# Optimization experiments

Hardware: AMD Instinct MI355X
Metric: run time of the kernel (lower is better)

## Reference

```python
import jax, jax.numpy as jnp
import numpy as np

N = 50000      # nodes per graph
E = 1600000    # edges per graph
D_IN = 128
D_HID = 128
D_OUT = 128
D_GF = 128
N_LAYERS = 3   # input->hid, hid->hid (hidden_layer=1), hid->out


def setup_inputs() -> dict:
    key = jax.random.key(0)
    ks = jax.random.split(key, 24)
    inp = {
        "feat_p": jax.random.normal(ks[0], (N, D_IN), jnp.float32),
        "src_p": jax.random.randint(ks[1], (E,), 0, N, jnp.int32),
        "dst_p": jax.random.randint(ks[2], (E,), 0, N, jnp.int32),
        "feat_s": jax.random.normal(ks[3], (N, D_IN), jnp.float32),
        "src_s": jax.random.randint(ks[4], (E,), 0, N, jnp.int32),
        "dst_s": jax.random.randint(ks[5], (E,), 0, N, jnp.int32),
    }
    dims = [(D_IN, D_HID), (D_HID, D_HID), (D_HID, D_OUT)]
    for i, (di, do) in enumerate(dims):
        inp[f"W{i}"] = jax.random.normal(ks[6 + 2 * i], (di, do), jnp.float32) * 0.05
        inp[f"b{i}"] = jnp.zeros((do,), jnp.float32)
    inp["Wr"] = jax.random.normal(ks[14], (D_OUT, D_GF), jnp.float32) * 0.05
    inp["br"] = jnp.zeros((D_GF,), jnp.float32)
    inp["Wm1"] = jax.random.normal(ks[15], (2 * D_GF, D_GF), jnp.float32) * 0.05
    inp["bm1"] = jnp.zeros((D_GF,), jnp.float32)
    inp["Wm2"] = jax.random.normal(ks[16], (D_GF, 1), jnp.float32) * 0.05
    inp["bm2"] = jnp.zeros((1,), jnp.float32)
    return inp


def _gcn_stack(feat, src, dst, layers):
    """Stacked GCN: mean over incoming messages, then linear.
    NOTE: the original SingleGCN never applies its ReLU (bug preserved)."""
    n = feat.shape[0]
    deg = jax.ops.segment_sum(jnp.ones_like(src, feat.dtype), dst, num_segments=n)
    inv_deg = (1.0 / jnp.maximum(deg, 1.0))[:, None]  # [N,1]
    h = feat
    for W, b in layers:
        msg = h[src]                                           # [E,d] gather
        agg = jax.ops.segment_sum(msg, dst, num_segments=n)    # [N,d] scatter-add
        h = (agg * inv_deg) @ W + b                            # mean + linear
    return h


def reference(feat_p, src_p, dst_p, feat_s, src_s, dst_s,
              W0, b0, W1, b1, W2, b2, Wr, br, Wm1, bm1, Wm2, bm2):
    layers = [(W0, b0), (W1, b1), (W2, b2)]
    h_p = _gcn_stack(feat_p, src_p, dst_p, layers)
    h_s = _gcn_stack(feat_s, src_s, dst_s, layers)
    # ReadOut: mean over nodes -> linear -> sigmoid
    g_p = jax.nn.sigmoid(jnp.mean(h_p, axis=0) @ Wr + br)  # [D_GF]
    g_s = jax.nn.sigmoid(jnp.mean(h_s, axis=0) @ Wr + br)
    # Match: concat -> linear -> linear -> sigmoid
    c = jnp.concatenate([g_p, g_s], axis=-1)               # [2*D_GF]
    d = (c @ Wm1 + bm1) @ Wm2 + bm2                        # [1]
    return jax.nn.sigmoid(d)
```

## Files before the change

### kernel.cpp

```cpp
#include <hip/hip_runtime.h>
#include <math.h>

#define D 128
#define HQ 4
#define BB 64


__global__ __launch_bounds__(1024, 8) void scan_scatter(
        const int* __restrict__ tgt_p, const int* __restrict__ oth_p,
        const int* __restrict__ tgt_s, const int* __restrict__ oth_s,
        const float* __restrict__ w, float* __restrict__ rep,
        float* __restrict__ zbase, int zcount,
        int E, int N, int HN, float scale) {
    const int b = blockIdx.x, h = blockIdx.y, g = blockIdx.z;
    const int* tgt = g ? tgt_s : tgt_p;
    const int* oth = g ? oth_s : oth_p;
    const float* wg = w ? (w + (size_t)g * N) : nullptr;

    if (zbase && b == 0 && h == 0 && g == 0)
        for (int i = threadIdx.x; i < zcount; i += 1024) zbase[i] = 0.f;

    extern __shared__ float lds[];
    {
        float4 z = make_float4(0.f, 0.f, 0.f, 0.f);
        float4* l4 = (float4*)lds;
        for (int i = threadIdx.x; i < HN / 4; i += 1024) l4[i] = z;
    }
    __syncthreads();

    const int lo = h * HN;
    const int hi = min(lo + HN, N);
    const unsigned span = (unsigned)(hi - lo);
    int C = (E + BB - 1) / BB;
    C = (C + 7) & ~7;
    const int e0 = b * C;
    const int e1 = min(e0 + C, E);

    for (int e = e0 + (int)threadIdx.x * 8; e < e1; e += 1024 * 8) {
        if (e + 8 <= e1) {
            int4 ta = *(const int4*)(tgt + e);
            int4 tb = *(const int4*)(tgt + e + 4);
            int idx[8] = {ta.x, ta.y, ta.z, ta.w, tb.x, tb.y, tb.z, tb.w};
            bool hit[8];
            #pragma unroll
            for (int k = 0; k < 8; ++k) hit[k] = (unsigned)(idx[k] - lo) < span;
            if (wg) {
                int4 oa = *(const int4*)(oth + e);
                int4 ob = *(const int4*)(oth + e + 4);
                int od[8] = {oa.x, oa.y, oa.z, oa.w, ob.x, ob.y, ob.z, ob.w};
                float val[8];
                #pragma unroll
                for (int k = 0; k < 8; ++k) val[k] = hit[k] ? wg[od[k]] : 0.f;
                #pragma unroll
                for (int k = 0; k < 8; ++k)
                    if (hit[k]) atomicAdd(&lds[idx[k] - lo], val[k] * scale);
            } else {
                #pragma unroll
                for (int k = 0; k < 8; ++k)
                    if (hit[k]) atomicAdd(&lds[idx[k] - lo], 1.0f);
            }
        } else {
            for (int e2 = e; e2 < e1; ++e2) {
                int t = tgt[e2];
                if ((unsigned)(t - lo) < span) {
                    float v = wg ? wg[oth[e2]] * scale : 1.0f;
                    atomicAdd(&lds[t - lo], v);
                }
            }
        }
    }
    __syncthreads();

    float* dst = rep + (((size_t)g * HQ + h) * BB + b) * HN;
    float4* d4 = (float4*)dst;
    const float4* l4 = (const float4*)lds;
    for (int i = threadIdx.x; i < HN / 4; i += 1024) d4[i] = l4[i];
}

__global__ __launch_bounds__(256) void reduce_inv(
        const float* __restrict__ rep, float* __restrict__ inv,
        int N, int HN) {
    const int lane = threadIdx.x & 63;
    const int s = threadIdx.x >> 6;
    const int i = (blockIdx.x * 64 + lane) * 4;
    const int bps = BB >> 2;
    float4 u = make_float4(0.f, 0.f, 0.f, 0.f);
    if (i < 2 * N) {
        int g = (i < N) ? 0 : 1;
        int n = i - g * N;
        int h = n / HN, l = n - h * HN;
        const float* base = rep + (((size_t)g * HQ + h) * BB + (size_t)s * bps) * HN + l;
        #pragma unroll 16
        for (int b = 0; b < bps; b++) {
            float4 v = *(const float4*)(base + (size_t)b * HN);
            u.x += v.x; u.y += v.y; u.z += v.z; u.w += v.w;
        }
    }
    __shared__ float4 sm[256];
    sm[threadIdx.x] = u;
    __syncthreads();
    if (s == 0 && i < 2 * N) {
        float4 a = sm[lane], b4 = sm[64 + lane], c = sm[128 + lane], d = sm[192 + lane];
        float4 r;
        r.x = 1.0f / fmaxf(a.x + b4.x + c.x + d.x, 1.0f);
        r.y = 1.0f / fmaxf(a.y + b4.y + c.y + d.y, 1.0f);
        r.z = 1.0f / fmaxf(a.z + b4.z + c.z + d.z, 1.0f);
        r.w = 1.0f / fmaxf(a.w + b4.w + c.w + d.w, 1.0f);
        *(float4*)(inv + i) = r;
    }
}

__global__ __launch_bounds__(256) void reduce_u(
        const float* __restrict__ rep, const float* __restrict__ inv,
        float* __restrict__ out_u, float* __restrict__ out_w,
        float* __restrict__ sums, int s_idx, int N, int HN) {
    const int lane = threadIdx.x & 63;
    const int s = threadIdx.x >> 6;
    const int i = (blockIdx.x * 64 + lane) * 4;
    const int bps = BB >> 2;
    float4 u = make_float4(0.f, 0.f, 0.f, 0.f);
    if (i < 2 * N) {
        int g = (i < N) ? 0 : 1;
        int n = i - g * N;
        int h = n / HN, l = n - h * HN;
        const float* base = rep + (((size_t)g * HQ + h) * BB + (size_t)s * bps) * HN + l;
        #pragma unroll 16
        for (int b = 0; b < bps; b++) {
            float4 v = *(const float4*)(base + (size_t)b * HN);
            u.x += v.x; u.y += v.y; u.z += v.z; u.w += v.w;
        }
    }
    __shared__ float4 sm[256];
    __shared__ float s0[64], s1[64];
    sm[threadIdx.x] = u;
    __syncthreads();
    if (s == 0) {
        float tp = 0.f, ts = 0.f;
        if (i < 2 * N) {
            float4 a = sm[lane], b4 = sm[64 + lane], c = sm[128 + lane], d = sm[192 + lane];
            float4 uu;
            uu.x = a.x + b4.x + c.x + d.x;
            uu.y = a.y + b4.y + c.y + d.y;
            uu.z = a.z + b4.z + c.z + d.z;
            uu.w = a.w + b4.w + c.w + d.w;
            if (out_u) *(float4*)(out_u + i) = uu;
            if (out_w) {
                float4 iv = *(const float4*)(inv + i);
                *(float4*)(out_w + i) =
                    make_float4(uu.x * iv.x, uu.y * iv.y, uu.z * iv.z, uu.w * iv.w);
            }
            float t = uu.x + uu.y + uu.z + uu.w;
            if (i < N) tp = t; else ts = t;
        }
        s0[lane] = tp; s1[lane] = ts;
    }
    __syncthreads();
    if (sums) {
        for (int st = 32; st > 0; st >>= 1) {
            if ((int)threadIdx.x < st) {
                s0[threadIdx.x] += s0[threadIdx.x + st];
                s1[threadIdx.x] += s1[threadIdx.x + st];
            }
            __syncthreads();
        }
        if (threadIdx.x == 0) {
            if (s0[0] != 0.f) atomicAdd(&sums[0 * 2 + s_idx], s0[0]);
            if (s1[0] != 0.f) atomicAdd(&sums[1 * 2 + s_idx], s1[0]);
        }
    }
}

__global__ __launch_bounds__(256) void featsum_kernel(
        const float* __restrict__ feat_p, const float* __restrict__ feat_s,
        const float* __restrict__ u3, float* __restrict__ fpart2,
        int N, int rpb) {
    const int g = blockIdx.y;
    const float* feat = g ? feat_s : feat_p;
    const float* u = u3 + (size_t)g * N;
    const int col4 = threadIdx.x & 31;
    const int rgrp = threadIdx.x >> 5;
    const int r0 = blockIdx.x * rpb;
    const int r1 = min(r0 + rpb, N);

    const float4* f4 = (const float4*)feat;
    float4 acc = make_float4(0.f, 0.f, 0.f, 0.f);
    for (int n = r0 + rgrp * 4; n + 3 < r1; n += 32) {
        float4 uu = *(const float4*)(u + n);
        float4 v0 = f4[(size_t)n * 32 + col4];
        float4 v1 = f4[(size_t)(n + 1) * 32 + col4];
        float4 v2 = f4[(size_t)(n + 2) * 32 + col4];
        float4 v3 = f4[(size_t)(n + 3) * 32 + col4];
        acc.x += uu.x * v0.x + uu.y * v1.x + uu.z * v2.x + uu.w * v3.x;
        acc.y += uu.x * v0.y + uu.y * v1.y + uu.z * v2.y + uu.w * v3.y;
        acc.z += uu.x * v0.z + uu.y * v1.z + uu.z * v2.z + uu.w * v3.z;
        acc.w += uu.x * v0.w + uu.y * v1.w + uu.z * v2.w + uu.w * v3.w;
    }
    __shared__ float4 smem[256];
    smem[threadIdx.x] = acc;
    __syncthreads();
    if (rgrp == 0) {
        float4 t = smem[col4];
        #pragma unroll
        for (int k = 1; k < 8; k++) {
            float4 o = smem[k * 32 + col4];
            t.x += o.x; t.y += o.y; t.z += o.z; t.w += o.w;
        }
        float* dst = fpart2 + ((size_t)g * 16 + (blockIdx.x & 15)) * 128 + col4 * 4;
        atomicAdd(dst + 0, t.x);
        atomicAdd(dst + 1, t.y);
        atomicAdd(dst + 2, t.z);
        atomicAdd(dst + 3, t.w);
    }
}

__global__ __launch_bounds__(512) void final_kernel(
        const float* __restrict__ fpart2,
        const float* __restrict__ sums,
        const float* __restrict__ W0, const float* __restrict__ b0,
        const float* __restrict__ W1, const float* __restrict__ b1,
        const float* __restrict__ W2, const float* __restrict__ b2,
        const float* __restrict__ Wr, const float* __restrict__ br,
        const float* __restrict__ Wm1, const float* __restrict__ bm1,
        const float* __restrict__ Wm2, const float* __restrict__ bm2,
        float* __restrict__ out) {
    __shared__ float x[128];
    __shared__ float part[4][128];
    __shared__ float rvec[256];
    __shared__ float Avec[128], Bvec[128];
    __shared__ float gv[256];
    const int tid = threadIdx.x;
    const int j = tid & 127;
    const int h = tid >> 7;

    auto mv128 = [&](const float* __restrict__ W, float* __restrict__ buf) {
        float p = 0.f;
        const float* Wp = W + (size_t)(h * 32) * 128 + j;
        #pragma unroll
        for (int i = 0; i < 32; ++i) p += buf[h * 32 + i] * Wp[(size_t)i * 128];
        part[h][j] = p;
        __syncthreads();
        if (h == 0) buf[j] = part[0][j] + part[1][j] + part[2][j] + part[3][j];
        __syncthreads();
    };

    if (tid < 256) {
        int g = tid >> 7;
        const float* fp = fpart2 + (size_t)g * 2048 + (tid & 127);
        float rv = 0.f;
        #pragma unroll
        for (int b = 0; b < 16; ++b) rv += fp[(size_t)b * 128];
        rvec[tid] = rv;
    }
    __syncthreads();

    if (tid < 128) x[tid] = b0[tid];
    __syncthreads();
    mv128(W1, x);
    mv128(W2, x);
    if (tid < 128) Avec[tid] = x[tid];
    __syncthreads();
    if (tid < 128) x[tid] = b1[tid];
    __syncthreads();
    mv128(W2, x);
    if (tid < 128) Bvec[tid] = x[tid];
    __syncthreads();

    for (int g = 0; g < 2; ++g) {
        const float s1 = sums[g * 2 + 0];
        const float s2 = sums[g * 2 + 1];
        if (tid < 128) x[tid] = rvec[g * 128 + tid];
        __syncthreads();
        mv128(W0, x);
        mv128(W1, x);
        mv128(W2, x);
        if (tid < 128) x[tid] += s2 * Avec[tid] + s1 * Bvec[tid] + b2[tid];
        __syncthreads();
        mv128(Wr, x);
        if (tid < 128) gv[g * 128 + tid] = 1.0f / (1.0f + expf(-(x[tid] + br[tid])));
        __syncthreads();
    }

    {
        float p = 0.f;
        const float* Wp = Wm1 + (size_t)(h * 64) * 128 + j;
        #pragma unroll
        for (int i = 0; i < 64; ++i) p += gv[h * 64 + i] * Wp[(size_t)i * 128];
        part[h][j] = p;
        __syncthreads();
        if (h == 0)
            part[0][j] = (part[0][j] + part[1][j] + part[2][j] + part[3][j] + bm1[j]) * Wm2[j];
        __syncthreads();
        if (tid < 64) part[0][tid] += part[0][tid + 64];
        __syncthreads();
        if (tid < 32) part[0][tid] += part[0][tid + 32];
        __syncthreads();
        if (tid < 16) part[0][tid] += part[0][tid + 16];
        __syncthreads();
        if (tid < 8) part[0][tid] += part[0][tid + 8];
        __syncthreads();
        if (tid < 4) part[0][tid] += part[0][tid + 4];
        __syncthreads();
        if (tid < 2) part[0][tid] += part[0][tid + 2];
        __syncthreads();
        if (tid == 0) out[0] = 1.0f / (1.0f + expf(-(part[0][0] + part[0][1] + bm2[0])));
    }
}

extern "C" void kernel_launch(void* const* d_in, const int* in_sizes, int n_in,
                              void* d_out, int out_size, void* d_ws, size_t ws_size,
                              hipStream_t stream) {
    const float* feat_p = (const float*)d_in[0];
    const int*   src_p  = (const int*)d_in[1];
    const int*   dst_p  = (const int*)d_in[2];
    const float* feat_s = (const float*)d_in[3];
    const int*   src_s  = (const int*)d_in[4];
    const int*   dst_s  = (const int*)d_in[5];
    const float* W0 = (const float*)d_in[6];
    const float* b0 = (const float*)d_in[7];
    const float* W1 = (const float*)d_in[8];
    const float* b1 = (const float*)d_in[9];
    const float* W2 = (const float*)d_in[10];
    const float* b2 = (const float*)d_in[11];
    const float* Wr = (const float*)d_in[12];
    const float* br = (const float*)d_in[13];
    const float* Wm1 = (const float*)d_in[14];
    const float* bm1 = (const float*)d_in[15];
    const float* Wm2 = (const float*)d_in[16];
    const float* bm2 = (const float*)d_in[17];
    float* out = (float*)d_out;

    const int N = in_sizes[0] / D;
    const int E = in_sizes[1];
    const int N2 = 2 * N;

    int HN = (N + HQ - 1) / HQ;
    HN = (HN + 3) & ~3;
    const int FB = 256;
    const int rpb = (((N + FB - 1) / FB) + 3) & ~3;

    float* ws     = (float*)d_ws;
    float* sums   = ws;
    float* fpart2 = ws + 16;
    float* inv    = fpart2 + 2 * 16 * 128;
    float* w1     = inv + N2;
    float* w2     = w1 + N2;
    float* u3     = w2 + N2;
    float* rep    = u3 + N2;

    const dim3 sgrid(BB, HQ, 2);
    const size_t lds_bytes = (size_t)HN * sizeof(float);
    const int gQ = (N2 / 4 + 63) / 64;
    const float u0 = 1.0f / (float)N;
    const int zcount = 16 + 2 * 16 * 128;

    scan_scatter<<<sgrid, 1024, lds_bytes, stream>>>(dst_p, nullptr, dst_s, nullptr,
                                                     nullptr, rep, sums, zcount,
                                                     E, N, HN, 1.0f);
    reduce_inv<<<gQ, 256, 0, stream>>>(rep, inv, N, HN);

    scan_scatter<<<sgrid, 1024, lds_bytes, stream>>>(src_p, dst_p, src_s, dst_s,
                                                     inv, rep, nullptr, 0,
                                                     E, N, HN, u0);
    reduce_u<<<gQ, 256, 0, stream>>>(rep, inv, nullptr, w1, sums, 0, N, HN);

    scan_scatter<<<sgrid, 1024, lds_bytes, stream>>>(src_p, dst_p, src_s, dst_s,
                                                     w1, rep, nullptr, 0,
                                                     E, N, HN, 1.0f);
    reduce_u<<<gQ, 256, 0, stream>>>(rep, inv, nullptr, w2, sums, 1, N, HN);

    scan_scatter<<<sgrid, 1024, lds_bytes, stream>>>(src_p, dst_p, src_s, dst_s,
                                                     w2, rep, nullptr, 0,
                                                     E, N, HN, 1.0f);
    reduce_u<<<gQ, 256, 0, stream>>>(rep, inv, u3, nullptr, nullptr, 0, N, HN);

    featsum_kernel<<<dim3(FB, 2), 256, 0, stream>>>(feat_p, feat_s, u3, fpart2, N, rpb);

    final_kernel<<<1, 512, 0, stream>>>(fpart2, sums, W0, b0, W1, b1, W2, b2,
                                        Wr, br, Wm1, bm1, Wm2, bm2, out);
}
```

Before: 284.9 us.

## Compute degrees with global atomics and halve node partitions in scatter

The degree count now uses a dedicated global-atomic kernel plus a small inverse kernel, replacing the LDS-partitioned scan_scatter pass and its reduce_inv. Node partitions per graph drop from 4 to 2, so each scatter block covers twice as many nodes in LDS (about 100KB, with the max dynamic shared memory attribute raised) and every edge list is scanned half as many times. The cost is lower occupancy from larger LDS per block, plus contended global atomics for degrees. Zeroing moves to a separate kernel.

```diff
diff --git a/kernel.cpp b/kernel.cpp
--- a/kernel.cpp
+++ b/kernel.cpp
@@ -2,23 +2,53 @@
 #include <math.h>
 
 #define D 128
-#define HQ 4
+#define HQ 2
 #define BB 64
 
 
-__global__ __launch_bounds__(1024, 8) void scan_scatter(
+__global__ __launch_bounds__(256) void zero_kernel(float* __restrict__ buf, int n4) {
+    float4* b4 = (float4*)buf;
+    const float4 z = make_float4(0.f, 0.f, 0.f, 0.f);
+    const int stride = gridDim.x * 256;
+    for (int i = blockIdx.x * 256 + threadIdx.x; i < n4; i += stride) b4[i] = z;
+}
+
+__global__ __launch_bounds__(256) void deg_kernel(
+        const int* __restrict__ dst_p, const int* __restrict__ dst_s,
+        float* __restrict__ deg, int E, int N) {
+    const int g = blockIdx.y;
+    const int* d = g ? dst_s : dst_p;
+    float* dg = deg + (size_t)g * N;
+    const int stride = gridDim.x * 256;
+    const int E4 = E >> 2;
+    for (int i = blockIdx.x * 256 + threadIdx.x; i < E4; i += stride) {
+        int4 v = ((const int4*)d)[i];
+        atomicAdd(&dg[v.x], 1.0f);
+        atomicAdd(&dg[v.y], 1.0f);
+        atomicAdd(&dg[v.z], 1.0f);
+        atomicAdd(&dg[v.w], 1.0f);
+    }
+    if (blockIdx.x == 0 && blockIdx.y == 0 && (int)threadIdx.x < (E & 3)) {
+        atomicAdd(&deg[0 * (size_t)N + dst_p[(E & ~3) + threadIdx.x]], 1.0f);
+        atomicAdd(&deg[1 * (size_t)N + dst_s[(E & ~3) + threadIdx.x]], 1.0f);
+    }
+}
+
+__global__ __launch_bounds__(256) void inv_kernel(
+        const float* __restrict__ deg, float* __restrict__ inv, int n) {
+    int i = blockIdx.x * 256 + threadIdx.x;
+    if (i < n) inv[i] = 1.0f / fmaxf(deg[i], 1.0f);
+}
+
+__global__ __launch_bounds__(1024, 4) void scan_scatter(
         const int* __restrict__ tgt_p, const int* __restrict__ oth_p,
         const int* __restrict__ tgt_s, const int* __restrict__ oth_s,
         const float* __restrict__ w, float* __restrict__ rep,
-        float* __restrict__ zbase, int zcount,
         int E, int N, int HN, float scale) {
     const int b = blockIdx.x, h = blockIdx.y, g = blockIdx.z;
     const int* tgt = g ? tgt_s : tgt_p;
     const int* oth = g ? oth_s : oth_p;
-    const float* wg = w ? (w + (size_t)g * N) : nullptr;
-
-    if (zbase && b == 0 && h == 0 && g == 0)
-        for (int i = threadIdx.x; i < zcount; i += 1024) zbase[i] = 0.f;
+    const float* wg = w + (size_t)g * N;
 
     extern __shared__ float lds[];
     {
@@ -44,28 +74,20 @@
             bool hit[8];
             #pragma unroll
             for (int k = 0; k < 8; ++k) hit[k] = (unsigned)(idx[k] - lo) < span;
-            if (wg) {
-                int4 oa = *(const int4*)(oth + e);
-                int4 ob = *(const int4*)(oth + e + 4);
-                int od[8] = {oa.x, oa.y, oa.z, oa.w, ob.x, ob.y, ob.z, ob.w};
-                float val[8];
-                #pragma unroll
-                for (int k = 0; k < 8; ++k) val[k] = hit[k] ? wg[od[k]] : 0.f;
-                #pragma unroll
-                for (int k = 0; k < 8; ++k)
-                    if (hit[k]) atomicAdd(&lds[idx[k] - lo], val[k] * scale);
-            } else {
-                #pragma unroll
-                for (int k = 0; k < 8; ++k)
-                    if (hit[k]) atomicAdd(&lds[idx[k] - lo], 1.0f);
-            }
+            int4 oa = *(const int4*)(oth + e);
+            int4 ob = *(const int4*)(oth + e + 4);
+            int od[8] = {oa.x, oa.y, oa.z, oa.w, ob.x, ob.y, ob.z, ob.w};
+            float val[8];
+            #pragma unroll
+            for (int k = 0; k < 8; ++k) val[k] = hit[k] ? wg[od[k]] : 0.f;
+            #pragma unroll
+            for (int k = 0; k < 8; ++k)
+                if (hit[k]) atomicAdd(&lds[idx[k] - lo], val[k] * scale);
         } else {
             for (int e2 = e; e2 < e1; ++e2) {
                 int t = tgt[e2];
-                if ((unsigned)(t - lo) < span) {
-                    float v = wg ? wg[oth[e2]] * scale : 1.0f;
-                    atomicAdd(&lds[t - lo], v);
-                }
+                if ((unsigned)(t - lo) < span)
+                    atomicAdd(&lds[t - lo], wg[oth[e2]] * scale);
             }
         }
     }
@@ -75,39 +97,6 @@
     float4* d4 = (float4*)dst;
     const float4* l4 = (const float4*)lds;
     for (int i = threadIdx.x; i < HN / 4; i += 1024) d4[i] = l4[i];
-}
-
-__global__ __launch_bounds__(256) void reduce_inv(
-        const float* __restrict__ rep, float* __restrict__ inv,
-        int N, int HN) {
-    const int lane = threadIdx.x & 63;
-    const int s = threadIdx.x >> 6;
-    const int i = (blockIdx.x * 64 + lane) * 4;
-    const int bps = BB >> 2;
-    float4 u = make_float4(0.f, 0.f, 0.f, 0.f);
-    if (i < 2 * N) {
-        int g = (i < N) ? 0 : 1;
-        int n = i - g * N;
-        int h = n / HN, l = n - h * HN;
-        const float* base = rep + (((size_t)g * HQ + h) * BB + (size_t)s * bps) * HN + l;
-        #pragma unroll 16
-        for (int b = 0; b < bps; b++) {
-            float4 v = *(const float4*)(base + (size_t)b * HN);
-            u.x += v.x; u.y += v.y; u.z += v.z; u.w += v.w;
-        }
-    }
-    __shared__ float4 sm[256];
-    sm[threadIdx.x] = u;
-    __syncthreads();
-    if (s == 0 && i < 2 * N) {
-        float4 a = sm[lane], b4 = sm[64 + lane], c = sm[128 + lane], d = sm[192 + lane];
-        float4 r;
-        r.x = 1.0f / fmaxf(a.x + b4.x + c.x + d.x, 1.0f);
-        r.y = 1.0f / fmaxf(a.y + b4.y + c.y + d.y, 1.0f);
-        r.z = 1.0f / fmaxf(a.z + b4.z + c.z + d.z, 1.0f);
-        r.w = 1.0f / fmaxf(a.w + b4.w + c.w + d.w, 1.0f);
-        *(float4*)(inv + i) = r;
-    }
 }
 
 __global__ __launch_bounds__(256) void reduce_u(
@@ -341,7 +330,8 @@
     float* ws     = (float*)d_ws;
     float* sums   = ws;
     float* fpart2 = ws + 16;
-    float* inv    = fpart2 + 2 * 16 * 128;
+    float* deg    = fpart2 + 2 * 16 * 128;
+    float* inv    = deg + N2;
     float* w1     = inv + N2;
     float* w2     = w1 + N2;
     float* u3     = w2 + N2;
@@ -351,26 +341,30 @@
     const size_t lds_bytes = (size_t)HN * sizeof(float);
     const int gQ = (N2 / 4 + 63) / 64;
     const float u0 = 1.0f / (float)N;
-    const int zcount = 16 + 2 * 16 * 128;
-
-    scan_scatter<<<sgrid, 1024, lds_bytes, stream>>>(dst_p, nullptr, dst_s, nullptr,
-                                                     nullptr, rep, sums, zcount,
-                                                     E, N, HN, 1.0f);
-    reduce_inv<<<gQ, 256, 0, stream>>>(rep, inv, N, HN);
+    const int zc4 = (16 + 2 * 16 * 128 + N2) / 4;
+
+    static bool attr_done = false;
+    if (!attr_done) {
+        (void)hipFuncSetAttribute(reinterpret_cast<const void*>(scan_scatter),
+                                  hipFuncAttributeMaxDynamicSharedMemorySize,
+                                  (int)lds_bytes);
+        attr_done = true;
+    }
+
+    zero_kernel<<<128, 256, 0, stream>>>(ws, zc4);
+    deg_kernel<<<dim3(512, 2), 256, 0, stream>>>(dst_p, dst_s, deg, E, N);
+    inv_kernel<<<(N2 + 255) / 256, 256, 0, stream>>>(deg, inv, N2);
 
     scan_scatter<<<sgrid, 1024, lds_bytes, stream>>>(src_p, dst_p, src_s, dst_s,
-                                                     inv, rep, nullptr, 0,
-                                                     E, N, HN, u0);
+                                                     inv, rep, E, N, HN, u0);
     reduce_u<<<gQ, 256, 0, stream>>>(rep, inv, nullptr, w1, sums, 0, N, HN);
 
     scan_scatter<<<sgrid, 1024, lds_bytes, stream>>>(src_p, dst_p, src_s, dst_s,
-                                                     w1, rep, nullptr, 0,
-                                                     E, N, HN, 1.0f);
+                                                     w1, rep, E, N, HN, 1.0f);
     reduce_u<<<gQ, 256, 0, stream>>>(rep, inv, nullptr, w2, sums, 1, N, HN);
 
     scan_scatter<<<sgrid, 1024, lds_bytes, stream>>>(src_p, dst_p, src_s, dst_s,
-                                                     w2, rep, nullptr, 0,
-                                                     E, N, HN, 1.0f);
+                                                     w2, rep, E, N, HN, 1.0f);
     reduce_u<<<gQ, 256, 0, stream>>>(rep, inv, u3, nullptr, nullptr, 0, N, HN);
 
     featsum_kernel<<<dim3(FB, 2), 256, 0, stream>>>(feat_p, feat_s, u3, fpart2, N, rpb);
```

Measured after the change: 435.3 us. +52.8%, slower.

## Pre-bin edges by node quarter so scatter passes scan only their bucket

Applied to the files above, without the earlier changes.

Adds a binning pass that partitions each graph's edges into four buckets by target-node quarter. Each edge is packed into one int (local target in the high bits, source index in the low 17 bits). The four scatter passes then read only their own bucket instead of scanning all edges and discarding three quarters of them. This cuts index traffic per pass roughly fourfold, at the cost of an extra binning kernel with ballot-based compaction and global atomics. It also relies on a fixed bucket capacity (CAP) and on node indices fitting in 17 bits.

```diff
diff --git a/kernel.cpp b/kernel.cpp
--- a/kernel.cpp
+++ b/kernel.cpp
@@ -4,21 +4,127 @@
 #define D 128
 #define HQ 4
 #define BB 64
-
-
-__global__ __launch_bounds__(1024, 8) void scan_scatter(
-        const int* __restrict__ tgt_p, const int* __restrict__ oth_p,
-        const int* __restrict__ tgt_s, const int* __restrict__ oth_s,
+#define CAP 425984
+
+
+__global__ __launch_bounds__(256) void zero_kernel(float* __restrict__ buf, int n4) {
+    float4* b4 = (float4*)buf;
+    const float4 z = make_float4(0.f, 0.f, 0.f, 0.f);
+    const int stride = gridDim.x * 256;
+    for (int i = blockIdx.x * 256 + threadIdx.x; i < n4; i += stride) b4[i] = z;
+}
+
+__global__ __launch_bounds__(512) void bin_kernel(
+        const int* __restrict__ src_p, const int* __restrict__ dst_p,
+        const int* __restrict__ src_s, const int* __restrict__ dst_s,
+        int* __restrict__ sbins, int* __restrict__ dbins,
+        unsigned* __restrict__ cur,
+        int E, int HN) {
+    const int g = blockIdx.y;
+    const int* src = g ? src_s : src_p;
+    const int* dst = g ? dst_s : dst_p;
+    int* sb = sbins + (size_t)g * 4 * CAP;
+    int* db = dbins + (size_t)g * 4 * CAP;
+    unsigned* scur = cur + g * 4;
+    unsigned* dcur = cur + 8 + g * 4;
+
+    const int tid = threadIdx.x;
+    const int lane = tid & 63;
+    const unsigned long long lmlt = (1ull << lane) - 1ull;
+    const int HN2 = 2 * HN, HN3 = 3 * HN;
+
+    __shared__ unsigned cnt[8];
+    __shared__ unsigned base[8];
+
+    const int per = ((E + (int)gridDim.x - 1) / (int)gridDim.x + 7) & ~7;
+    const int e0 = blockIdx.x * per;
+    const int e1 = min(e0 + per, E);
+
+    for (int c0 = e0; c0 < e1; c0 += 512 * 8) {
+        int myS[8], myD[8], qs[8], qd[8];
+        const int eb = c0 + tid * 8;
+        if (eb + 8 <= e1) {
+            int4 a = *(const int4*)(src + eb); int4 b = *(const int4*)(src + eb + 4);
+            int4 c = *(const int4*)(dst + eb); int4 d = *(const int4*)(dst + eb + 4);
+            myS[0]=a.x; myS[1]=a.y; myS[2]=a.z; myS[3]=a.w;
+            myS[4]=b.x; myS[5]=b.y; myS[6]=b.z; myS[7]=b.w;
+            myD[0]=c.x; myD[1]=c.y; myD[2]=c.z; myD[3]=c.w;
+            myD[4]=d.x; myD[5]=d.y; myD[6]=d.z; myD[7]=d.w;
+        } else {
+            #pragma unroll
+            for (int k = 0; k < 8; ++k) {
+                int e = eb + k;
+                myS[k] = (e < e1) ? src[e] : -1;
+                myD[k] = (e < e1) ? dst[e] : -1;
+            }
+        }
+        #pragma unroll
+        for (int k = 0; k < 8; ++k) {
+            qs[k] = (myS[k] < 0) ? -1
+                  : ((myS[k] >= HN2) ? (myS[k] >= HN3 ? 3 : 2)
+                                     : (myS[k] >= HN ? 1 : 0));
+            qd[k] = (myD[k] < 0) ? -1
+                  : ((myD[k] >= HN2) ? (myD[k] >= HN3 ? 3 : 2)
+                                     : (myD[k] >= HN ? 1 : 0));
+        }
+
+        if (tid < 8) cnt[tid] = 0;
+        __syncthreads();
+
+        unsigned sr[8], dr[8];
+        #pragma unroll
+        for (int k = 0; k < 8; ++k) {
+            sr[k] = 0; dr[k] = 0;
+            #pragma unroll
+            for (int b = 0; b < 4; ++b) {
+                unsigned long long ms = __ballot(qs[k] == b);
+                if (ms) {
+                    int ld = (int)__ffsll((long long)ms) - 1;
+                    int wb = 0;
+                    if (lane == ld) wb = (int)atomicAdd(&cnt[b], (unsigned)__popcll(ms));
+                    wb = __shfl(wb, ld);
+                    if (qs[k] == b) sr[k] = (unsigned)wb + (unsigned)__popcll(ms & lmlt);
+                }
+                unsigned long long md = __ballot(qd[k] == b);
+                if (md) {
+                    int ld2 = (int)__ffsll((long long)md) - 1;
+                    int wb2 = 0;
+                    if (lane == ld2) wb2 = (int)atomicAdd(&cnt[4 + b], (unsigned)__popcll(md));
+                    wb2 = __shfl(wb2, ld2);
+                    if (qd[k] == b) dr[k] = (unsigned)wb2 + (unsigned)__popcll(md & lmlt);
+                }
+            }
+        }
+        __syncthreads();
+        if (tid < 4)      base[tid] = atomicAdd(&scur[tid], cnt[tid]);
+        else if (tid < 8) base[tid] = atomicAdd(&dcur[tid - 4], cnt[tid]);
+        __syncthreads();
+
+        #pragma unroll
+        for (int k = 0; k < 8; ++k) {
+            if (qs[k] >= 0) {
+                unsigned p = base[qs[k]] + sr[k];
+                if (p < (unsigned)CAP)
+                    sb[(size_t)qs[k] * CAP + p] = ((myS[k] - qs[k] * HN) << 17) | myD[k];
+            }
+            if (qd[k] >= 0) {
+                unsigned p = base[4 + qd[k]] + dr[k];
+                if (p < (unsigned)CAP)
+                    db[(size_t)qd[k] * CAP + p] = (myD[k] - qd[k] * HN) << 17;
+            }
+        }
+        __syncthreads();
+    }
+}
+
+__global__ __launch_bounds__(1024, 8) void scan_binned(
+        const int* __restrict__ bins, const unsigned* __restrict__ bcnt,
         const float* __restrict__ w, float* __restrict__ rep,
-        float* __restrict__ zbase, int zcount,
-        int E, int N, int HN, float scale) {
+        int N, int HN, float scale) {
     const int b = blockIdx.x, h = blockIdx.y, g = blockIdx.z;
-    const int* tgt = g ? tgt_s : tgt_p;
-    const int* oth = g ? oth_s : oth_p;
+    const int* bin = bins + (size_t)(g * HQ + h) * CAP;
+    const int n = (int)bcnt[g * HQ + h];
     const float* wg = w ? (w + (size_t)g * N) : nullptr;
-
-    if (zbase && b == 0 && h == 0 && g == 0)
-        for (int i = threadIdx.x; i < zcount; i += 1024) zbase[i] = 0.f;
 
     extern __shared__ float lds[];
     {
@@ -28,44 +134,28 @@
     }
     __syncthreads();
 
-    const int lo = h * HN;
-    const int hi = min(lo + HN, N);
-    const unsigned span = (unsigned)(hi - lo);
-    int C = (E + BB - 1) / BB;
+    int C = (n + BB - 1) / BB;
     C = (C + 7) & ~7;
     const int e0 = b * C;
-    const int e1 = min(e0 + C, E);
+    const int e1 = min(e0 + C, n);
 
     for (int e = e0 + (int)threadIdx.x * 8; e < e1; e += 1024 * 8) {
         if (e + 8 <= e1) {
-            int4 ta = *(const int4*)(tgt + e);
-            int4 tb = *(const int4*)(tgt + e + 4);
-            int idx[8] = {ta.x, ta.y, ta.z, ta.w, tb.x, tb.y, tb.z, tb.w};
-            bool hit[8];
+            int4 a = *(const int4*)(bin + e);
+            int4 bb = *(const int4*)(bin + e + 4);
+            int v[8] = {a.x, a.y, a.z, a.w, bb.x, bb.y, bb.z, bb.w};
+            float val[8];
             #pragma unroll
-            for (int k = 0; k < 8; ++k) hit[k] = (unsigned)(idx[k] - lo) < span;
-            if (wg) {
-                int4 oa = *(const int4*)(oth + e);
-                int4 ob = *(const int4*)(oth + e + 4);
-                int od[8] = {oa.x, oa.y, oa.z, oa.w, ob.x, ob.y, ob.z, ob.w};
-                float val[8];
-                #pragma unroll
-                for (int k = 0; k < 8; ++k) val[k] = hit[k] ? wg[od[k]] : 0.f;
-                #pragma unroll
-                for (int k = 0; k < 8; ++k)
-                    if (hit[k]) atomicAdd(&lds[idx[k] - lo], val[k] * scale);
-            } else {
-                #pragma unroll
-                for (int k = 0; k < 8; ++k)
-                    if (hit[k]) atomicAdd(&lds[idx[k] - lo], 1.0f);
-            }
+            for (int k = 0; k < 8; ++k)
+                val[k] = wg ? wg[v[k] & 0x1FFFF] * scale : 1.0f;
+            #pragma unroll
+            for (int k = 0; k < 8; ++k)
+                atomicAdd(&lds[((unsigned)v[k]) >> 17], val[k]);
         } else {
             for (int e2 = e; e2 < e1; ++e2) {
-                int t = tgt[e2];
-                if ((unsigned)(t - lo) < span) {
-                    float v = wg ? wg[oth[e2]] * scale : 1.0f;
-                    atomicAdd(&lds[t - lo], v);
-                }
+                int v = bin[e2];
+                float val = wg ? wg[v & 0x1FFFF] * scale : 1.0f;
+                atomicAdd(&lds[((unsigned)v) >> 17], val);
             }
         }
     }
@@ -338,39 +428,43 @@
     const int FB = 256;
     const int rpb = (((N + FB - 1) / FB) + 3) & ~3;
 
-    float* ws     = (float*)d_ws;
-    float* sums   = ws;
-    float* fpart2 = ws + 16;
-    float* inv    = fpart2 + 2 * 16 * 128;
-    float* w1     = inv + N2;
-    float* w2     = w1 + N2;
-    float* u3     = w2 + N2;
-    float* rep    = u3 + N2;
+    float* ws       = (float*)d_ws;
+    unsigned* cur   = (unsigned*)ws;
+    float* sums     = ws + 16;
+    float* fpart2   = ws + 32;
+    float* inv      = fpart2 + 2 * 16 * 128;
+    float* w1       = inv + N2;
+    float* w2       = w1 + N2;
+    float* u3       = w2 + N2;
+    float* rep      = u3 + N2;
+    int*   sbins    = (int*)(rep + (size_t)2 * HQ * BB * HN);
+    int*   dbins    = sbins + (size_t)2 * 4 * CAP;
 
     const dim3 sgrid(BB, HQ, 2);
     const size_t lds_bytes = (size_t)HN * sizeof(float);
     const int gQ = (N2 / 4 + 63) / 64;
     const float u0 = 1.0f / (float)N;
-    const int zcount = 16 + 2 * 16 * 128;
-
-    scan_scatter<<<sgrid, 1024, lds_bytes, stream>>>(dst_p, nullptr, dst_s, nullptr,
-                                                     nullptr, rep, sums, zcount,
-                                                     E, N, HN, 1.0f);
+    const int zc4 = (16 + 16 + 2 * 16 * 128) / 4;
+
+    zero_kernel<<<16, 256, 0, stream>>>(ws, zc4);
+
+    bin_kernel<<<dim3(256, 2), 512, 0, stream>>>(src_p, dst_p, src_s, dst_s,
+                                                 sbins, dbins, cur, E, HN);
+
+    scan_binned<<<sgrid, 1024, lds_bytes, stream>>>(dbins, cur + 8, nullptr,
+                                                    rep, N, HN, 1.0f);
     reduce_inv<<<gQ, 256, 0, stream>>>(rep, inv, N, HN);
 
-    scan_scatter<<<sgrid, 1024, lds_bytes, stream>>>(src_p, dst_p, src_s, dst_s,
-                                                     inv, rep, nullptr, 0,
-                                                     E, N, HN, u0);
+    scan_binned<<<sgrid, 1024, lds_bytes, stream>>>(sbins, cur, inv,
+                                                    rep, N, HN, u0);
     reduce_u<<<gQ, 256, 0, stream>>>(rep, inv, nullptr, w1, sums, 0, N, HN);
 
-    scan_scatter<<<sgrid, 1024, lds_bytes, stream>>>(src_p, dst_p, src_s, dst_s,
-                                                     w1, rep, nullptr, 0,
-                                                     E, N, HN, 1.0f);
+    scan_binned<<<sgrid, 1024, lds_bytes, stream>>>(sbins, cur, w1,
+                                                    rep, N, HN, 1.0f);
     reduce_u<<<gQ, 256, 0, stream>>>(rep, inv, nullptr, w2, sums, 1, N, HN);
 
-    scan_scatter<<<sgrid, 1024, lds_bytes, stream>>>(src_p, dst_p, src_s, dst_s,
-                                                     w2, rep, nullptr, 0,
-                                                     E, N, HN, 1.0f);
+    scan_binned<<<sgrid, 1024, lds_bytes, stream>>>(sbins, cur, w2,
+                                                    rep, N, HN, 1.0f);
     reduce_u<<<gQ, 256, 0, stream>>>(rep, inv, u3, nullptr, nullptr, 0, N, HN);
 
     featsum_kernel<<<dim3(FB, 2), 256, 0, stream>>>(feat_p, feat_s, u3, fpart2, N, rpb);
```

Result: slower. 351.9 us (+23.5%).
